# Kernel tuning notes

Hardware: AMD Instinct MI355X
Metric: run time of the kernel (lower is better)

Reference implementation:

```python
import jax, jax.numpy as jnp
import numpy as np

KH, KW = 3, 3  # spatial kernel from kernel_size=(1,3,3,C)


def _extract_patches_valid(x, kh, kw):
    # TF extract_image_patches ordering: depth = (row, col, channel) flattened.
    B, H, W, C = x.shape
    Ho, Wo = H - kh + 1, W - kw + 1
    # stack kh*kw shifted views -> [B, Ho, Wo, kh*kw, C]
    views = [x[:, i:i + Ho, j:j + Wo, :] for i in range(kh) for j in range(kw)]
    patches = jnp.stack(views, axis=3)
    return patches.reshape(B, Ho, Wo, kh * kw * C)


def setup_inputs() -> dict:
    key = jax.random.key(0)
    k1, k2, k3 = jax.random.split(key, 3)
    B, H, W, C = 32, 112, 112, 32
    filters = 128
    patch_dim = KH * KW * C  # 288
    x = jax.random.normal(k1, (B, H, W, C), dtype=jnp.float32)
    ccs = jax.random.uniform(k2, (patch_dim, filters), dtype=jnp.float32)  # RandomUniform(0,1)
    beta = jax.random.uniform(k3, (filters,), dtype=jnp.float32)
    return {"x": x, "ccs": ccs, "beta": beta}


def reference(x, ccs, beta):
    B = x.shape[0]
    patch_dim, filters = ccs.shape
    patches = _extract_patches_valid(x, KH, KW)  # [B, Ho, Wo, patch_dim]
    Ho, Wo = patches.shape[1], patches.shape[2]
    p = patches.reshape(B, Ho * Wo, patch_dim)  # [B, P, D]
    # squared distance: ||p||^2 - 2 p.ccs + ||ccs||^2  -> [B, P, filters]
    p_sq = jnp.sum(p * p, axis=2, keepdims=True)
    c_sq = jnp.sum(ccs * ccs, axis=0, keepdims=True)
    scores = p_sq - 2.0 * jnp.einsum('bpd,df->bpf', p, ccs) + c_sq
    out = jnp.exp(-beta * scores)  # RBF activation, beta broadcast over filters
    return out.reshape(B, Ho, Wo, filters)
```

## Files before the change

### kernel.cpp

```cpp
#include <hip/hip_runtime.h>


typedef __attribute__((ext_vector_type(8))) short bf16x8;
typedef __attribute__((ext_vector_type(4))) float f32x4;

#define HH 112
#define WW 112
#define CC 32
#define HO 110
#define WO 110
#define NF 128
#define KD 288
#define RPX 114
#define XP 32
#define CSP 116
#define ORPB 2
#define SROWS 4

__device__ __forceinline__ unsigned short f32_to_bf16(float f) {
    unsigned u = __float_as_uint(f);
    unsigned r = u + 0x7FFFu + ((u >> 16) & 1u);
    return (unsigned short)(r >> 16);
}

__global__ __launch_bounds__(256) void rbf_prologue(const float* __restrict__ ccs,
                                                    unsigned short* __restrict__ ccs_t,
                                                    float* __restrict__ c_sq) {
    int idx = blockIdx.x * 256 + threadIdx.x;
    int d = idx >> 7;
    int f = idx & 127;
    ccs_t[f * KD + d] = f32_to_bf16(ccs[idx]);
    if (blockIdx.x == 0 && threadIdx.x < 128) {
        const int fc = threadIdx.x;
        float s = 0.f;
        #pragma unroll 8
        for (int dd = 0; dd < KD; ++dd) {
            float v = ccs[dd * NF + fc];
            s += v * v;
        }
        c_sq[fc] = s;
    }
}

__global__ __launch_bounds__(256) void rbf_main(const float* __restrict__ x,
                                                const unsigned short* __restrict__ ccs_t,
                                                const float* __restrict__ c_sq,
                                                const float* __restrict__ beta,
                                                float* __restrict__ out) {
    __shared__ unsigned short xs[SROWS * RPX * XP];
    __shared__ float colsum[SROWS * CSP];
    __shared__ float p_sq[ORPB * 112];

    const int t = threadIdx.x;
    const int y0 = blockIdx.x * ORPB;
    const int b = blockIdx.y;

    const int lane  = t & 63;
    const int wave  = t >> 6;
    const int laneM = lane & 15;
    const int quad  = lane >> 4;
    const int pl    = laneM & 1;

    #pragma unroll
    for (int p = 0; p < 14; ++p) {
        int idx = t + p * 256;
        int q = idx & 7;
        int ic = idx >> 3;
        int col = ic % 112;
        int i = ic / 112;
        const float4 v = *(const float4*)(x + ((size_t)(b * HH + y0 + i) * WW + col) * CC + q * 4);
        unsigned short h0 = f32_to_bf16(v.x), h1 = f32_to_bf16(v.y);
        unsigned short h2 = f32_to_bf16(v.z), h3 = f32_to_bf16(v.w);
        uint2 pk;
        pk.x = (unsigned)h0 | ((unsigned)h1 << 16);
        pk.y = (unsigned)h2 | ((unsigned)h3 << 16);
        *(uint2*)(&xs[(i * RPX + col) * XP + q * 4]) = pk;
        float part = v.x * v.x + v.y * v.y + v.z * v.z + v.w * v.w;
        part += __shfl_xor(part, 1);
        part += __shfl_xor(part, 2);
        part += __shfl_xor(part, 4);
        if (q == 0) colsum[i * CSP + col] = part;
    }
    __syncthreads();

    if (t < ORPB * 112) {
        int r = t / 112;
        int c = t - r * 112;
        float s = 0.f;
        #pragma unroll
        for (int i = 0; i < 3; ++i)
            #pragma unroll
            for (int j = 0; j < 3; ++j)
                s += colsum[(r + i) * CSP + c + j];
        p_sq[t] = s;
    }
    __syncthreads();

    const unsigned short* ap0 = ccs_t + (size_t)(wave * 32 + laneM) * KD + quad * 8;
    const unsigned short* ap1 = ap0 + 16 * KD;

    const int fb = wave * 32 + quad * 4;
    const float4 cs0 = *(const float4*)(c_sq + fb);
    const float4 cs1 = *(const float4*)(c_sq + fb + 16);
    const float4 bt0 = *(const float4*)(beta + fb);
    const float4 bt1 = *(const float4*)(beta + fb + 16);

    for (int r = 0; r < ORPB; ++r) {
        f32x4 acc[7][2];
        #pragma unroll
        for (int mi = 0; mi < 7; ++mi) {
            acc[mi][0] = (f32x4){0.f, 0.f, 0.f, 0.f};
            acc[mi][1] = (f32x4){0.f, 0.f, 0.f, 0.f};
        }

        #pragma unroll
        for (int kb = 0; kb < 9; ++kb) {
            const int ki = kb / 3, kj = kb % 3;
            bf16x8 a0 = *(const bf16x8*)(ap0 + kb * 32);
            bf16x8 a1 = *(const bf16x8*)(ap1 + kb * 32);
            #pragma unroll
            for (int mi = 0; mi < 7; ++mi) {
                const bf16x8 bf = *(const bf16x8*)(&xs[((r + ki) * RPX + mi * 16 + laneM + kj) * XP + quad * 8]);
                acc[mi][0] = __builtin_amdgcn_mfma_f32_16x16x32_bf16(a0, bf, acc[mi][0], 0, 0, 0);
                acc[mi][1] = __builtin_amdgcn_mfma_f32_16x16x32_bf16(a1, bf, acc[mi][1], 0, 0, 0);
            }
        }

        float* orow = out + (size_t)((b * HO + y0 + r) * WO) * NF;
        #pragma unroll
        for (int mi = 0; mi < 7; ++mi) {
            const int px = mi * 16 + laneM;
            const float ps = p_sq[r * 112 + px];
            f32x4 o0, o1;
            o0[0] = __expf(-bt0.x * (ps - 2.f * acc[mi][0][0] + cs0.x));
            o0[1] = __expf(-bt0.y * (ps - 2.f * acc[mi][0][1] + cs0.y));
            o0[2] = __expf(-bt0.z * (ps - 2.f * acc[mi][0][2] + cs0.z));
            o0[3] = __expf(-bt0.w * (ps - 2.f * acc[mi][0][3] + cs0.w));
            o1[0] = __expf(-bt1.x * (ps - 2.f * acc[mi][1][0] + cs1.x));
            o1[1] = __expf(-bt1.y * (ps - 2.f * acc[mi][1][1] + cs1.y));
            o1[2] = __expf(-bt1.z * (ps - 2.f * acc[mi][1][2] + cs1.z));
            o1[3] = __expf(-bt1.w * (ps - 2.f * acc[mi][1][3] + cs1.w));

            f32x4 sendv = pl ? o0 : o1;
            f32x4 recv;
            recv[0] = __shfl_xor(sendv[0], 1);
            recv[1] = __shfl_xor(sendv[1], 1);
            recv[2] = __shfl_xor(sendv[2], 1);
            recv[3] = __shfl_xor(sendv[3], 1);
            const f32x4 v1 = pl ? recv : o0;
            const f32x4 v2 = pl ? o1 : recv;

            const int pxe = mi * 16 + (laneM & ~1);
            float* op1 = orow + (size_t)pxe * NF + fb + pl * 16;
            if (pxe < WO)
                *(f32x4*)op1 = v1;
            if (pxe + 1 < WO)
                *(f32x4*)(op1 + NF) = v2;
        }
    }
}

extern "C" void kernel_launch(void* const* d_in, const int* in_sizes, int n_in,
                              void* d_out, int out_size, void* d_ws, size_t ws_size,
                              hipStream_t stream) {
    const float* x    = (const float*)d_in[0];
    const float* ccs  = (const float*)d_in[1];
    const float* beta = (const float*)d_in[2];
    float* out = (float*)d_out;

    unsigned short* ccs_t = (unsigned short*)d_ws;
    float* c_sq = (float*)((char*)d_ws + 128 * KD * sizeof(unsigned short));

    rbf_prologue<<<144, 256, 0, stream>>>(ccs, ccs_t, c_sq);
    rbf_main<<<dim3(55, 32), 256, 0, stream>>>(x, ccs_t, c_sq, beta, out);
}
```

Baseline: 282.2 us.

## Double block to 512 threads, split pixel tiles across wave pairs, nontemporal stores

Raises the workgroup from 4 to 8 waves. Each filter group is now handled by two waves that split the 7 pixel tiles (4 vs 3) by parity, which gives more waves per block to hide MFMA and LDS latency and cuts per-wave accumulator registers. Output stores become nontemporal to avoid polluting the cache with the write-only output. The 4/3 split leaves the waves unevenly loaded, and the A-fragment loads from global memory are now duplicated across the wave pairs.

Measured after the change: 275.4 us. -2.4%, faster.

```diff
diff --git a/kernel.cpp b/kernel.cpp
--- a/kernel.cpp
+++ b/kernel.cpp
@@ -42,7 +42,72 @@
     }
 }
 
-__global__ __launch_bounds__(256) void rbf_main(const float* __restrict__ x,
+template<int NMI, int MIP>
+__device__ __forceinline__ void compute_rows(const unsigned short* __restrict__ xs,
+                                             const float* __restrict__ p_sq,
+                                             const unsigned short* __restrict__ ap0,
+                                             const unsigned short* __restrict__ ap1,
+                                             int laneM, int quad, int pl, int fb,
+                                             float4 cs0, float4 cs1, float4 bt0, float4 bt1,
+                                             float* __restrict__ out, int b, int y0) {
+    for (int r = 0; r < ORPB; ++r) {
+        f32x4 acc[NMI][2];
+        #pragma unroll
+        for (int j = 0; j < NMI; ++j) {
+            acc[j][0] = (f32x4){0.f, 0.f, 0.f, 0.f};
+            acc[j][1] = (f32x4){0.f, 0.f, 0.f, 0.f};
+        }
+
+        #pragma unroll
+        for (int kb = 0; kb < 9; ++kb) {
+            const int ki = kb / 3, kj = kb % 3;
+            bf16x8 a0 = *(const bf16x8*)(ap0 + kb * 32);
+            bf16x8 a1 = *(const bf16x8*)(ap1 + kb * 32);
+            #pragma unroll
+            for (int j = 0; j < NMI; ++j) {
+                const int mi = 2 * j + MIP;
+                const bf16x8 bf = *(const bf16x8*)(&xs[((r + ki) * RPX + mi * 16 + laneM + kj) * XP + quad * 8]);
+                acc[j][0] = __builtin_amdgcn_mfma_f32_16x16x32_bf16(a0, bf, acc[j][0], 0, 0, 0);
+                acc[j][1] = __builtin_amdgcn_mfma_f32_16x16x32_bf16(a1, bf, acc[j][1], 0, 0, 0);
+            }
+        }
+
+        float* orow = out + (size_t)((b * HO + y0 + r) * WO) * NF;
+        #pragma unroll
+        for (int j = 0; j < NMI; ++j) {
+            const int mi = 2 * j + MIP;
+            const int px = mi * 16 + laneM;
+            const float ps = p_sq[r * 112 + px];
+            f32x4 o0, o1;
+            o0[0] = __expf(-bt0.x * (ps - 2.f * acc[j][0][0] + cs0.x));
+            o0[1] = __expf(-bt0.y * (ps - 2.f * acc[j][0][1] + cs0.y));
+            o0[2] = __expf(-bt0.z * (ps - 2.f * acc[j][0][2] + cs0.z));
+            o0[3] = __expf(-bt0.w * (ps - 2.f * acc[j][0][3] + cs0.w));
+            o1[0] = __expf(-bt1.x * (ps - 2.f * acc[j][1][0] + cs1.x));
+            o1[1] = __expf(-bt1.y * (ps - 2.f * acc[j][1][1] + cs1.y));
+            o1[2] = __expf(-bt1.z * (ps - 2.f * acc[j][1][2] + cs1.z));
+            o1[3] = __expf(-bt1.w * (ps - 2.f * acc[j][1][3] + cs1.w));
+
+            f32x4 sendv = pl ? o0 : o1;
+            f32x4 recv;
+            recv[0] = __shfl_xor(sendv[0], 1);
+            recv[1] = __shfl_xor(sendv[1], 1);
+            recv[2] = __shfl_xor(sendv[2], 1);
+            recv[3] = __shfl_xor(sendv[3], 1);
+            const f32x4 v1 = pl ? recv : o0;
+            const f32x4 v2 = pl ? o1 : recv;
+
+            const int pxe = mi * 16 + (laneM & ~1);
+            float* op1 = orow + (size_t)pxe * NF + fb + pl * 16;
+            if (pxe < WO)
+                __builtin_nontemporal_store(v1, (f32x4*)op1);
+            if (pxe + 1 < WO)
+                __builtin_nontemporal_store(v2, (f32x4*)(op1 + NF));
+        }
+    }
+}
+
+__global__ __launch_bounds__(512) void rbf_main(const float* __restrict__ x,
                                                 const unsigned short* __restrict__ ccs_t,
                                                 const float* __restrict__ c_sq,
                                                 const float* __restrict__ beta,
@@ -57,13 +122,15 @@
 
     const int lane  = t & 63;
     const int wave  = t >> 6;
+    const int wgrp  = wave & 3;
+    const int mipar = wave >> 2;
     const int laneM = lane & 15;
     const int quad  = lane >> 4;
     const int pl    = laneM & 1;
 
     #pragma unroll
-    for (int p = 0; p < 14; ++p) {
-        int idx = t + p * 256;
+    for (int p = 0; p < 7; ++p) {
+        int idx = t + p * 512;
         int q = idx & 7;
         int ic = idx >> 3;
         int col = ic % 112;
@@ -96,68 +163,19 @@
     }
     __syncthreads();
 
-    const unsigned short* ap0 = ccs_t + (size_t)(wave * 32 + laneM) * KD + quad * 8;
+    const unsigned short* ap0 = ccs_t + (size_t)(wgrp * 32 + laneM) * KD + quad * 8;
     const unsigned short* ap1 = ap0 + 16 * KD;
 
-    const int fb = wave * 32 + quad * 4;
+    const int fb = wgrp * 32 + quad * 4;
     const float4 cs0 = *(const float4*)(c_sq + fb);
     const float4 cs1 = *(const float4*)(c_sq + fb + 16);
     const float4 bt0 = *(const float4*)(beta + fb);
     const float4 bt1 = *(const float4*)(beta + fb + 16);
 
-    for (int r = 0; r < ORPB; ++r) {
-        f32x4 acc[7][2];
-        #pragma unroll
-        for (int mi = 0; mi < 7; ++mi) {
-            acc[mi][0] = (f32x4){0.f, 0.f, 0.f, 0.f};
-            acc[mi][1] = (f32x4){0.f, 0.f, 0.f, 0.f};
-        }
-
-        #pragma unroll
-        for (int kb = 0; kb < 9; ++kb) {
-            const int ki = kb / 3, kj = kb % 3;
-            bf16x8 a0 = *(const bf16x8*)(ap0 + kb * 32);
-            bf16x8 a1 = *(const bf16x8*)(ap1 + kb * 32);
-            #pragma unroll
-            for (int mi = 0; mi < 7; ++mi) {
-                const bf16x8 bf = *(const bf16x8*)(&xs[((r + ki) * RPX + mi * 16 + laneM + kj) * XP + quad * 8]);
-                acc[mi][0] = __builtin_amdgcn_mfma_f32_16x16x32_bf16(a0, bf, acc[mi][0], 0, 0, 0);
-                acc[mi][1] = __builtin_amdgcn_mfma_f32_16x16x32_bf16(a1, bf, acc[mi][1], 0, 0, 0);
-            }
-        }
-
-        float* orow = out + (size_t)((b * HO + y0 + r) * WO) * NF;
-        #pragma unroll
-        for (int mi = 0; mi < 7; ++mi) {
-            const int px = mi * 16 + laneM;
-            const float ps = p_sq[r * 112 + px];
-            f32x4 o0, o1;
-            o0[0] = __expf(-bt0.x * (ps - 2.f * acc[mi][0][0] + cs0.x));
-            o0[1] = __expf(-bt0.y * (ps - 2.f * acc[mi][0][1] + cs0.y));
-            o0[2] = __expf(-bt0.z * (ps - 2.f * acc[mi][0][2] + cs0.z));
-            o0[3] = __expf(-bt0.w * (ps - 2.f * acc[mi][0][3] + cs0.w));
-            o1[0] = __expf(-bt1.x * (ps - 2.f * acc[mi][1][0] + cs1.x));
-            o1[1] = __expf(-bt1.y * (ps - 2.f * acc[mi][1][1] + cs1.y));
-            o1[2] = __expf(-bt1.z * (ps - 2.f * acc[mi][1][2] + cs1.z));
-            o1[3] = __expf(-bt1.w * (ps - 2.f * acc[mi][1][3] + cs1.w));
-
-            f32x4 sendv = pl ? o0 : o1;
-            f32x4 recv;
-            recv[0] = __shfl_xor(sendv[0], 1);
-            recv[1] = __shfl_xor(sendv[1], 1);
-            recv[2] = __shfl_xor(sendv[2], 1);
-            recv[3] = __shfl_xor(sendv[3], 1);
-            const f32x4 v1 = pl ? recv : o0;
-            const f32x4 v2 = pl ? o1 : recv;
-
-            const int pxe = mi * 16 + (laneM & ~1);
-            float* op1 = orow + (size_t)pxe * NF + fb + pl * 16;
-            if (pxe < WO)
-                *(f32x4*)op1 = v1;
-            if (pxe + 1 < WO)
-                *(f32x4*)(op1 + NF) = v2;
-        }
-    }
+    if (mipar == 0)
+        compute_rows<4, 0>(xs, p_sq, ap0, ap1, laneM, quad, pl, fb, cs0, cs1, bt0, bt1, out, b, y0);
+    else
+        compute_rows<3, 1>(xs, p_sq, ap0, ap1, laneM, quad, pl, fb, cs0, cs1, bt0, bt1, out, b, y0);
 }
 
 extern "C" void kernel_launch(void* const* d_in, const int* in_sizes, int n_in,
@@ -172,5 +190,5 @@
     float* c_sq = (float*)((char*)d_ws + 128 * KD * sizeof(unsigned short));
 
     rbf_prologue<<<144, 256, 0, stream>>>(ccs, ccs_t, c_sq);
-    rbf_main<<<dim3(55, 32), 256, 0, stream>>>(x, ccs_t, c_sq, beta, out);
+    rbf_main<<<dim3(55, 32), 512, 0, stream>>>(x, ccs_t, c_sq, beta, out);
 }
```

## Precompute bf16 input and patch norms in separate passes; read B operand from global

Applied to the files above, without the earlier changes.

Adds two pre-pass kernels that convert x to bf16 once and compute per-pixel column and patch squared norms into workspace. The main kernel then reads its B fragments straight from global/L2 instead of staging in LDS, which removes the per-block redundant conversion of overlapping rows and the two block barriers. Output stores become nontemporal in both paths. This costs extra launches and a full extra write and read of a bf16 copy of x. The old LDS path is kept as a fallback when the workspace is too small.

After: 329.8 us. +16.9%, slower.

```diff
diff --git a/kernel.cpp b/kernel.cpp
--- a/kernel.cpp
+++ b/kernel.cpp
@@ -11,10 +11,10 @@
 #define WO 110
 #define NF 128
 #define KD 288
+#define ORPB 2
 #define RPX 114
 #define XP 32
 #define CSP 116
-#define ORPB 2
 #define SROWS 4
 
 __device__ __forceinline__ unsigned short f32_to_bf16(float f) {
@@ -42,11 +42,138 @@
     }
 }
 
-__global__ __launch_bounds__(256) void rbf_main(const float* __restrict__ x,
-                                                const unsigned short* __restrict__ ccs_t,
-                                                const float* __restrict__ c_sq,
-                                                const float* __restrict__ beta,
-                                                float* __restrict__ out) {
+__global__ __launch_bounds__(256) void rbf_pre_x(const float* __restrict__ x,
+                                                 unsigned short* __restrict__ xbf,
+                                                 float* __restrict__ colsum) {
+    const int t = threadIdx.x;
+    const int r0 = blockIdx.x * 4;
+    const int b  = blockIdx.y;
+    #pragma unroll
+    for (int p = 0; p < 14; ++p) {
+        int idx = t + p * 256;
+        int q = idx & 7;
+        int ic = idx >> 3;
+        int col = ic % 112;
+        int i = ic / 112;
+        const size_t e = ((size_t)(b * HH + r0 + i) * WW + col) * CC + q * 4;
+        const float4 v = *(const float4*)(x + e);
+        unsigned short h0 = f32_to_bf16(v.x), h1 = f32_to_bf16(v.y);
+        unsigned short h2 = f32_to_bf16(v.z), h3 = f32_to_bf16(v.w);
+        uint2 pk;
+        pk.x = (unsigned)h0 | ((unsigned)h1 << 16);
+        pk.y = (unsigned)h2 | ((unsigned)h3 << 16);
+        *(uint2*)(xbf + e) = pk;
+        float part = v.x * v.x + v.y * v.y + v.z * v.z + v.w * v.w;
+        part += __shfl_xor(part, 1);
+        part += __shfl_xor(part, 2);
+        part += __shfl_xor(part, 4);
+        if (q == 0) colsum[(size_t)(b * HH + r0 + i) * WW + col] = part;
+    }
+}
+
+__global__ __launch_bounds__(256) void rbf_pre_psq(const float* __restrict__ colsum,
+                                                   float* __restrict__ p_sq) {
+    int idx = blockIdx.x * 256 + threadIdx.x;
+    int px = idx % 112;
+    int y  = (idx / 112) % 110;
+    int b  = idx / (112 * 110);
+    int c0 = (px > 109) ? 109 : px;
+    float s = 0.f;
+    #pragma unroll
+    for (int i = 0; i < 3; ++i) {
+        const float* row = colsum + (size_t)(b * HH + y + i) * WW + c0;
+        s += row[0] + row[1] + row[2];
+    }
+    p_sq[idx] = s;
+}
+
+__global__ __launch_bounds__(256) void rbf_main_nb(const unsigned short* __restrict__ xbf,
+                                                   const unsigned short* __restrict__ ccs_t,
+                                                   const float* __restrict__ p_sq,
+                                                   const float* __restrict__ c_sq,
+                                                   const float* __restrict__ beta,
+                                                   float* __restrict__ out) {
+    const int t = threadIdx.x;
+    const int y0 = blockIdx.x * ORPB;
+    const int b  = blockIdx.y;
+
+    const int lane  = t & 63;
+    const int wave  = t >> 6;
+    const int laneM = lane & 15;
+    const int quad  = lane >> 4;
+    const int pl    = laneM & 1;
+
+    const unsigned short* ap0 = ccs_t + (size_t)(wave * 32 + laneM) * KD + quad * 8;
+    const unsigned short* ap1 = ap0 + 16 * KD;
+
+    const int fb = wave * 32 + quad * 4;
+    const float4 cs0 = *(const float4*)(c_sq + fb);
+    const float4 cs1 = *(const float4*)(c_sq + fb + 16);
+    const float4 bt0 = *(const float4*)(beta + fb);
+    const float4 bt1 = *(const float4*)(beta + fb + 16);
+
+    for (int r = 0; r < ORPB; ++r) {
+        f32x4 acc[7][2];
+        #pragma unroll
+        for (int mi = 0; mi < 7; ++mi) {
+            acc[mi][0] = (f32x4){0.f, 0.f, 0.f, 0.f};
+            acc[mi][1] = (f32x4){0.f, 0.f, 0.f, 0.f};
+        }
+
+        #pragma unroll
+        for (int kb = 0; kb < 9; ++kb) {
+            const int ki = kb / 3, kj = kb % 3;
+            bf16x8 a0 = *(const bf16x8*)(ap0 + kb * 32);
+            bf16x8 a1 = *(const bf16x8*)(ap1 + kb * 32);
+            const unsigned short* brow = xbf + ((size_t)(b * HH + y0 + r + ki) * WW + laneM + kj) * CC + quad * 8;
+            #pragma unroll
+            for (int mi = 0; mi < 7; ++mi) {
+                const bf16x8 bf = *(const bf16x8*)(brow + (size_t)mi * 16 * CC);
+                acc[mi][0] = __builtin_amdgcn_mfma_f32_16x16x32_bf16(a0, bf, acc[mi][0], 0, 0, 0);
+                acc[mi][1] = __builtin_amdgcn_mfma_f32_16x16x32_bf16(a1, bf, acc[mi][1], 0, 0, 0);
+            }
+        }
+
+        const float* psrow = p_sq + ((size_t)b * HO + y0 + r) * 112;
+        float* orow = out + (size_t)((b * HO + y0 + r) * WO) * NF;
+        #pragma unroll
+        for (int mi = 0; mi < 7; ++mi) {
+            const int px = mi * 16 + laneM;
+            const float ps = psrow[px];
+            f32x4 o0, o1;
+            o0[0] = __expf(-bt0.x * (ps - 2.f * acc[mi][0][0] + cs0.x));
+            o0[1] = __expf(-bt0.y * (ps - 2.f * acc[mi][0][1] + cs0.y));
+            o0[2] = __expf(-bt0.z * (ps - 2.f * acc[mi][0][2] + cs0.z));
+            o0[3] = __expf(-bt0.w * (ps - 2.f * acc[mi][0][3] + cs0.w));
+            o1[0] = __expf(-bt1.x * (ps - 2.f * acc[mi][1][0] + cs1.x));
+            o1[1] = __expf(-bt1.y * (ps - 2.f * acc[mi][1][1] + cs1.y));
+            o1[2] = __expf(-bt1.z * (ps - 2.f * acc[mi][1][2] + cs1.z));
+            o1[3] = __expf(-bt1.w * (ps - 2.f * acc[mi][1][3] + cs1.w));
+
+            f32x4 sendv = pl ? o0 : o1;
+            f32x4 recv;
+            recv[0] = __shfl_xor(sendv[0], 1);
+            recv[1] = __shfl_xor(sendv[1], 1);
+            recv[2] = __shfl_xor(sendv[2], 1);
+            recv[3] = __shfl_xor(sendv[3], 1);
+            const f32x4 v1 = pl ? recv : o0;
+            const f32x4 v2 = pl ? o1 : recv;
+
+            const int pxe = mi * 16 + (laneM & ~1);
+            float* op1 = orow + (size_t)pxe * NF + fb + pl * 16;
+            if (pxe < WO)
+                __builtin_nontemporal_store(v1, (f32x4*)op1);
+            if (pxe + 1 < WO)
+                __builtin_nontemporal_store(v2, (f32x4*)(op1 + NF));
+        }
+    }
+}
+
+__global__ __launch_bounds__(256) void rbf_main_lds(const float* __restrict__ x,
+                                                    const unsigned short* __restrict__ ccs_t,
+                                                    const float* __restrict__ c_sq,
+                                                    const float* __restrict__ beta,
+                                                    float* __restrict__ out) {
     __shared__ unsigned short xs[SROWS * RPX * XP];
     __shared__ float colsum[SROWS * CSP];
     __shared__ float p_sq[ORPB * 112];
@@ -98,7 +225,6 @@
 
     const unsigned short* ap0 = ccs_t + (size_t)(wave * 32 + laneM) * KD + quad * 8;
     const unsigned short* ap1 = ap0 + 16 * KD;
-
     const int fb = wave * 32 + quad * 4;
     const float4 cs0 = *(const float4*)(c_sq + fb);
     const float4 cs1 = *(const float4*)(c_sq + fb + 16);
@@ -112,7 +238,6 @@
             acc[mi][0] = (f32x4){0.f, 0.f, 0.f, 0.f};
             acc[mi][1] = (f32x4){0.f, 0.f, 0.f, 0.f};
         }
-
         #pragma unroll
         for (int kb = 0; kb < 9; ++kb) {
             const int ki = kb / 3, kj = kb % 3;
@@ -125,7 +250,6 @@
                 acc[mi][1] = __builtin_amdgcn_mfma_f32_16x16x32_bf16(a1, bf, acc[mi][1], 0, 0, 0);
             }
         }
-
         float* orow = out + (size_t)((b * HO + y0 + r) * WO) * NF;
         #pragma unroll
         for (int mi = 0; mi < 7; ++mi) {
@@ -140,7 +264,6 @@
             o1[1] = __expf(-bt1.y * (ps - 2.f * acc[mi][1][1] + cs1.y));
             o1[2] = __expf(-bt1.z * (ps - 2.f * acc[mi][1][2] + cs1.z));
             o1[3] = __expf(-bt1.w * (ps - 2.f * acc[mi][1][3] + cs1.w));
-
             f32x4 sendv = pl ? o0 : o1;
             f32x4 recv;
             recv[0] = __shfl_xor(sendv[0], 1);
@@ -149,13 +272,12 @@
             recv[3] = __shfl_xor(sendv[3], 1);
             const f32x4 v1 = pl ? recv : o0;
             const f32x4 v2 = pl ? o1 : recv;
-
             const int pxe = mi * 16 + (laneM & ~1);
             float* op1 = orow + (size_t)pxe * NF + fb + pl * 16;
             if (pxe < WO)
-                *(f32x4*)op1 = v1;
+                __builtin_nontemporal_store(v1, (f32x4*)op1);
             if (pxe + 1 < WO)
-                *(f32x4*)(op1 + NF) = v2;
+                __builtin_nontemporal_store(v2, (f32x4*)(op1 + NF));
         }
     }
 }
@@ -168,9 +290,26 @@
     const float* beta = (const float*)d_in[2];
     float* out = (float*)d_out;
 
-    unsigned short* ccs_t = (unsigned short*)d_ws;
-    float* c_sq = (float*)((char*)d_ws + 128 * KD * sizeof(unsigned short));
+    constexpr size_t OFF_CCS_T = 0;
+    constexpr size_t OFF_CSQ   = 73728;
+    constexpr size_t OFF_XBF   = 74240;
+    constexpr size_t OFF_CS    = 25764608;
+    constexpr size_t OFF_PSQ   = 27370240;
+    constexpr size_t WS_NEED   = 28947200;
+
+    unsigned short* ccs_t = (unsigned short*)((char*)d_ws + OFF_CCS_T);
+    float* c_sq = (float*)((char*)d_ws + OFF_CSQ);
 
     rbf_prologue<<<144, 256, 0, stream>>>(ccs, ccs_t, c_sq);
-    rbf_main<<<dim3(55, 32), 256, 0, stream>>>(x, ccs_t, c_sq, beta, out);
-}
+
+    if (ws_size >= WS_NEED) {
+        unsigned short* xbf = (unsigned short*)((char*)d_ws + OFF_XBF);
+        float* colsum = (float*)((char*)d_ws + OFF_CS);
+        float* p_sq   = (float*)((char*)d_ws + OFF_PSQ);
+        rbf_pre_x<<<dim3(28, 32), 256, 0, stream>>>(x, xbf, colsum);
+        rbf_pre_psq<<<1540, 256, 0, stream>>>(colsum, p_sq);
+        rbf_main_nb<<<dim3(55, 32), 256, 0, stream>>>(xbf, ccs_t, p_sq, c_sq, beta, out);
+    } else {
+        rbf_main_lds<<<dim3(55, 32), 256, 0, stream>>>(x, ccs_t, c_sq, beta, out);
+    }
+}
```
